# Kernel optimization log

Measured on AMD Instinct MI355X. Metric: run time of the kernel, lower is better.

## Reference

```python
import jax, jax.numpy as jnp
import numpy as np
from jax.scipy.linalg import solve_triangular

B, M, S, NBPS = 32768, 16, 8, 4
NUM_ITER = 2
EPS = 1e-4

def _pam_gray(b):
    if len(b) > 1:
        return (1 - 2 * b[0]) * (2 ** len(b[1:]) - _pam_gray(b[1:]))
    return 1 - 2 * b[0]

def _qam(nbps):
    n = 2 ** nbps
    pts = np.zeros(n, np.complex64)
    for i in range(n):
        b = np.array([int(c) for c in np.binary_repr(i, nbps)])
        pts[i] = _pam_gray(b[0::2]) + 1j * _pam_gray(b[1::2])
    pts = pts / np.sqrt(np.mean(np.abs(pts) ** 2))
    labels = ((np.arange(n)[:, None] >> np.arange(nbps - 1, -1, -1)) & 1).astype(np.float32)
    return pts.astype(np.complex64), labels

_PTS_NP, _LAB_NP = _qam(NBPS)
PTS = jnp.asarray(_PTS_NP)                                   # [P] complex64, unit-energy Gray QAM16
PTS_E = jnp.asarray((np.abs(_PTS_NP) ** 2).astype(np.float32))  # [P]
LAB = jnp.asarray(_LAB_NP)                                   # [P, K] bit labels (MSB first)
ASGN = 2.0 * LAB - 1.0                                       # [P, K], +1 where bit==1

def _symbol_logits(llr):
    # LLRs2SymbolLogits: llr=[...,S,K] (llr = log p(b=1)/p(b=0)) -> per-point log-prior [...,S,P]
    return jnp.sum(jax.nn.log_sigmoid(ASGN * llr[..., None, :]), axis=-1)

def _moments(logits):
    # SymbolLogits2Moments: softmax over points -> mean / variance of soft symbols
    p = jax.nn.softmax(logits, axis=-1)                       # [..., S, P]
    mean = jnp.einsum('...p,p->...', p.astype(jnp.complex64), PTS)
    e2 = jnp.einsum('...p,p->...', p, PTS_E)
    var = e2 - (mean.real ** 2 + mean.imag ** 2)
    return mean, var

def _demap(x_hat, llr_a, no_eff):
    # maxlog DemapperWithPrior, LLR = log p(b=1)/p(b=0)
    diff = x_hat[..., None] - PTS                             # [..., S, P]
    d2 = diff.real ** 2 + diff.imag ** 2
    exps = -d2 / no_eff[..., None] + _symbol_logits(llr_a)    # [..., S, P]
    e = exps[..., None]                                       # [..., S, P, 1]
    neg = jnp.float32(-1e30)
    l1 = jnp.max(jnp.where(LAB == 1.0, e, neg), axis=-2)      # [..., S, K]
    l0 = jnp.max(jnp.where(LAB == 0.0, e, neg), axis=-2)
    return l1 - l0

def _forward(y_re, y_im, h_re, h_im, prior, s_re, s_im):
    y = jax.lax.complex(y_re, y_im)                           # [B, M]
    h = jax.lax.complex(h_re, h_im)                           # [B, M, S]
    s = jax.lax.complex(s_re, s_im)                           # [B, M, M] Hermitian PSD
    # whiten_channel: s = L L^H, y <- L^-1 y, h <- L^-1 h
    L = jnp.linalg.cholesky(s)
    y = solve_triangular(L, y[..., None], lower=True)[..., 0]
    h = solve_triangular(L, h, lower=True)
    y_mf = jnp.einsum('bms,bm->bs', jnp.conj(h), y)[..., None]   # [B, S, 1] matched filter
    g = jnp.einsum('bmi,bmj->bij', jnp.conj(h), h)               # [B, S, S] Gram matrix
    # real-valued channel representation [[Re,-Im],[Im,Re]]
    hr = jnp.concatenate([
        jnp.concatenate([h.real, -h.imag], axis=-1),
        jnp.concatenate([h.imag, h.real], axis=-1)], axis=-2)    # [B, 2M, 2S]
    gr = jnp.einsum('bmi,bmj->bij', hr, hr)                      # [B, 2S, 2S]
    eye2s = jnp.eye(2 * S, dtype=jnp.float32)
    llr_d = prior
    llr_a = jnp.zeros_like(prior)
    for _ in range(NUM_ITER):
        llr_a = llr_d
        x_hat, var_x = _moments(_symbol_logits(llr_a))           # [B, S]
        # parallel interference cancellation in matched-filter domain
        y_mf_pic = (y_mf + g * x_hat[..., None, :]
                    - jnp.einsum('bij,bj->bi', g, x_hat)[..., None])  # [B, S, S]
        var2 = jnp.concatenate([var_x, var_x], axis=-1)          # [B, 2S]
        a = gr * var2[..., None, :] + eye2s                      # [B, 2S, 2S]
        a_inv = jnp.linalg.inv(a)
        mu = jnp.sum(a_inv * jnp.swapaxes(gr, -1, -2), axis=-1)  # diag(a_inv @ gr), [B, 2S]
        ypt = jnp.swapaxes(y_mf_pic, -1, -2)                     # [B, S, S] (stream-major)
        ypt_r = jnp.concatenate([ypt.real, ypt.imag], axis=-1)   # [B, S, 2S]
        ypt_r = jnp.concatenate([ypt_r, ypt_r], axis=-2)         # [B, 2S, 2S]
        z = jnp.sum(a_inv * ypt_r, axis=-1) / mu                 # [B, 2S] unbiased estimates
        zr, zi = jnp.split(z, 2, axis=-1)
        x_hat = jax.lax.complex(zr, zi)                          # [B, S]
        rho = mu / jnp.maximum(1.0 - var2 * mu, EPS)             # post-equalization SINR
        rho = jnp.split(rho, 2, axis=-1)[0]                      # [B, S]
        no_eff = 1.0 / rho
        llr_d = _demap(x_hat, llr_a, no_eff)
    return llr_d - llr_a  # extrinsic LLRs [B, S, K]

def setup_inputs() -> dict:
    key = jax.random.key(0)
    k = jax.random.split(key, 7)
    y_re = jax.random.normal(k[0], (B, M), jnp.float32)
    y_im = jax.random.normal(k[1], (B, M), jnp.float32)
    h_re = jax.random.normal(k[2], (B, M, S), jnp.float32) / np.float32(np.sqrt(2.0))
    h_im = jax.random.normal(k[3], (B, M, S), jnp.float32) / np.float32(np.sqrt(2.0))
    prior = 0.5 * jax.random.normal(k[4], (B, S, NBPS), jnp.float32)
    a = jax.lax.complex(jax.random.normal(k[5], (B, M, M), jnp.float32),
                        jax.random.normal(k[6], (B, M, M), jnp.float32)) / np.float32(np.sqrt(2.0 * M))
    s = jnp.einsum('bij,bkj->bik', a, jnp.conj(a)) + 0.5 * jnp.eye(M, dtype=jnp.complex64)
    return {"y_re": y_re, "y_im": y_im, "h_re": h_re, "h_im": h_im,
            "prior": prior, "s_re": s.real, "s_im": s.imag}

def reference(y_re, y_im, h_re, h_im, prior, s_re, s_im):
    return _forward(y_re, y_im, h_re, h_im, prior, s_re, s_im)
```

## Files before the change

### kernel.cpp

```cpp
#include <hip/hip_runtime.h>


#define EPS_F 1e-4f
#define INV_SQRT10 0.31622776601683794f
#define WSYNC() __builtin_amdgcn_wave_barrier()

__device__ __forceinline__ float rcpf(float x) { return __builtin_amdgcn_rcpf(x); }
__device__ __forceinline__ float pt_re(int p) {
    return (1.0f - 2.0f * (float)((p >> 3) & 1)) * (1.0f + 2.0f * (float)((p >> 1) & 1)) * INV_SQRT10;
}
__device__ __forceinline__ float pt_im(int p) {
    return (1.0f - 2.0f * (float)((p >> 2) & 1)) * (1.0f + 2.0f * (float)(p & 1)) * INV_SQRT10;
}

__global__ __launch_bounds__(64)
void mmse_pic_kernel(const float* __restrict__ y_re, const float* __restrict__ y_im,
                     const float* __restrict__ h_re, const float* __restrict__ h_im,
                     const float* __restrict__ prior,
                     const float* __restrict__ s_re, const float* __restrict__ s_im,
                     float* __restrict__ out)
{
    const int b = blockIdx.x, lane = threadIdx.x;
    const size_t bs = (size_t)b;

    __shared__ float2 Sc[16][28];
    __shared__ float2 Hc[16][10];
    __shared__ float2 xc_[8];
    __shared__ float2 ymc_[8];
    __shared__ float  vx_[8], ne_[8];
    __shared__ float  lsig[64];
    __shared__ float  logit_[8][20];
    __shared__ float  llrD_[8][4];

    {
        const float4* pr4 = (const float4*)(s_re + bs * 256);
        const float4* pi4 = (const float4*)(s_im + bs * 256);
        float4 vr = pr4[lane], vi = pi4[lane];
        int r = lane >> 2, c0 = (lane & 3) << 2;
        Sc[r][c0+0] = make_float2(vr.x, vi.x);
        Sc[r][c0+1] = make_float2(vr.y, vi.y);
        Sc[r][c0+2] = make_float2(vr.z, vi.z);
        Sc[r][c0+3] = make_float2(vr.w, vi.w);
        if (lane < 32) {
            const float4* hr4 = (const float4*)(h_re + bs * 128);
            const float4* hi4 = (const float4*)(h_im + bs * 128);
            float4 hr = hr4[lane], hi = hi4[lane];
            int row = lane >> 1, col = (lane & 1) << 2;
            float2 v0 = make_float2(hr.x, hi.x), v1 = make_float2(hr.y, hi.y);
            float2 v2 = make_float2(hr.z, hi.z), v3 = make_float2(hr.w, hi.w);
            Hc[row][col+0] = v0; Hc[row][col+1] = v1; Hc[row][col+2] = v2; Hc[row][col+3] = v3;
            Sc[row][16+col+0] = v0; Sc[row][16+col+1] = v1; Sc[row][16+col+2] = v2; Sc[row][16+col+3] = v3;
        }
        if (lane < 16) Sc[lane][24] = make_float2(y_re[bs*16+lane], y_im[bs*16+lane]);
        if (lane < 32) ((float*)llrD_)[lane] = prior[bs*32 + lane];
    }
    WSYNC();

    {
        const int j0 = lane & 15;
        for (int k = 0; k < 16; ++k) {
            float2 piv = Sc[k][k];
            float id = rcpf(piv.x*piv.x + piv.y*piv.y);
            float ipr = piv.x*id, ipi = -piv.y*id;
            int j1 = k + 1 + j0, j2 = j1 + 16;
            float2 rk0 = make_float2(0.f, 0.f), rk1 = make_float2(0.f, 0.f);
            if (j1 < 25) rk0 = Sc[k][j1];
            if (j2 < 25) rk1 = Sc[k][j2];
            #pragma unroll
            for (int p = 0; p < 4; ++p) {
                int i = (lane >> 4) + (p << 2);
                float2 aik = Sc[i][k];
                float mr = aik.x*ipr - aik.y*ipi;
                float mi = aik.x*ipi + aik.y*ipr;
                if (i == k) { mr = 0.f; mi = 0.f; }
                if (j1 < 25) {
                    float2 a = Sc[i][j1];
                    a.x -= mr*rk0.x - mi*rk0.y;
                    a.y -= mr*rk0.y + mi*rk0.x;
                    Sc[i][j1] = a;
                }
                if (j2 < 25) {
                    float2 a = Sc[i][j2];
                    a.x -= mr*rk1.x - mi*rk1.y;
                    a.y -= mr*rk1.y + mi*rk1.x;
                    Sc[i][j2] = a;
                }
            }
            WSYNC();
        }
    }
    {
        int i2 = lane >> 2, c = lane & 3;
        float2 d = Sc[i2][i2];
        float id = rcpf(d.x*d.x + d.y*d.y);
        float ipr = d.x*id, ipi = -d.y*id;
        #pragma unroll
        for (int q = 0; q < 3; ++q) {
            int j = 16 + c + (q << 2);
            if (j < 25) {
                float2 v = Sc[i2][j];
                Sc[i2][j] = make_float2(v.x*ipr - v.y*ipi, v.x*ipi + v.y*ipr);
            }
        }
    }
    WSYNC();

    const int s = lane >> 3, u = lane & 7;
    float g_re = 0.f, g_im = 0.f, ym_r = 0.f, ym_i = 0.f;
    #pragma unroll
    for (int m = 0; m < 16; ++m) {
        float2 h = Hc[m][s];
        float2 x = Sc[m][16 + u];
        float2 xy = Sc[m][24];
        g_re += h.x*x.x + h.y*x.y;
        g_im += h.x*x.y - h.y*x.x;
        ym_r += h.x*xy.x + h.y*xy.y;
        ym_i += h.x*xy.y - h.y*xy.x;
    }
    if (u == 0) ymc_[s] = make_float2(ym_r, ym_i);
    WSYNC();

    const float pr = pt_re(u), pi2 = pt_im(u), pe = pr*pr + pi2*pi2;
    float llr_a_reg = 0.f;

    for (int it = 0; it < 2; ++it) {
        {
            int ts = lane >> 3, tk = (lane >> 1) & 3, sg = lane & 1;
            float v = llrD_[ts][tk];
            float x = sg ? v : -v;
            lsig[lane] = fminf(x, 0.f) - log1pf(__expf(-fabsf(x)));
        }
        if (lane < 32) llr_a_reg = ((float*)llrD_)[lane];
        WSYNC();
        int base = s << 3;
        float lc = lsig[base | 2 | ((u >> 2) & 1)]
                 + lsig[base | 4 | ((u >> 1) & 1)]
                 + lsig[base | 6 | (u & 1)];
        float l0 = lc + lsig[base];
        float l1 = lc + lsig[base | 1];
        {
            float mx = fmaxf(l0, l1);
            mx = fmaxf(mx, __shfl_xor(mx, 1));
            mx = fmaxf(mx, __shfl_xor(mx, 2));
            mx = fmaxf(mx, __shfl_xor(mx, 4));
            float w0 = __expf(l0 - mx), w1 = __expf(l1 - mx);
            float a = w0 + w1, dw = w0 - w1;
            float se = a, mr = dw * pr, mi = a * pi2, e2 = a * pe;
            se += __shfl_xor(se,1); mr += __shfl_xor(mr,1); mi += __shfl_xor(mi,1); e2 += __shfl_xor(e2,1);
            se += __shfl_xor(se,2); mr += __shfl_xor(mr,2); mi += __shfl_xor(mi,2); e2 += __shfl_xor(e2,2);
            se += __shfl_xor(se,4); mr += __shfl_xor(mr,4); mi += __shfl_xor(mi,4); e2 += __shfl_xor(e2,4);
            if (u == 0) {
                float inv = rcpf(se);
                float mxr = mr*inv, mxi = mi*inv;
                xc_[s] = make_float2(mxr, mxi);
                vx_[s] = e2*inv - (mxr*mxr + mxi*mxi);
            }
        }
        WSYNC();
        float2 xj = xc_[u];
        float vj = vx_[u];
        float tr = g_re*xj.x - g_im*xj.y;
        float ti = g_re*xj.y + g_im*xj.x;
        tr += __shfl_xor(tr,1); ti += __shfl_xor(ti,1);
        tr += __shfl_xor(tr,2); ti += __shfl_xor(ti,2);
        tr += __shfl_xor(tr,4); ti += __shfl_xor(ti,4);
        float2 ym = ymc_[s];
        float br_ = ym.x - tr, bi_ = ym.y - ti;
        float Ar = g_re*vj + ((s == u) ? 1.f : 0.f);
        float Ai = g_im*vj;
        float Cr = g_re, Ci = g_im;
        #pragma unroll
        for (int k = 0; k < 8; ++k) {
            int rowsrc = (k << 3) | u;
            int colsrc = (s << 3) | k;
            float pvr = __shfl(Ar, k * 9);
            float pvi = __shfl(Ai, k * 9);
            float rAr = __shfl(Ar, rowsrc), rAi = __shfl(Ai, rowsrc);
            float rCr = __shfl(Cr, rowsrc), rCi = __shfl(Ci, rowsrc);
            float rbr = __shfl(br_, rowsrc), rbi = __shfl(bi_, rowsrc);
            float cAr = __shfl(Ar, colsrc), cAi = __shfl(Ai, colsrc);
            float id2 = rcpf(pvr*pvr + pvi*pvi);
            float ipr2 = pvr*id2, ipi2 = -pvi*id2;
            float mr2 = cAr*ipr2 - cAi*ipi2;
            float mi2 = cAr*ipi2 + cAi*ipr2;
            if (s == k) { mr2 = 0.f; mi2 = 0.f; }
            Ar  -= mr2*rAr - mi2*rAi;  Ai  -= mr2*rAi + mi2*rAr;
            Cr  -= mr2*rCr - mi2*rCi;  Ci  -= mr2*rCi + mi2*rCr;
            br_ -= mr2*rbr - mi2*rbi;  bi_ -= mr2*rbi + mi2*rbr;
        }
        if (s == u) {
            float id3 = rcpf(Ar*Ar + Ai*Ai);
            float ipr3 = Ar*id3, ipi3 = -Ai*id3;
            float wr = br_*ipr3 - bi_*ipi3;
            float wi = br_*ipi3 + bi_*ipr3;
            float ccr = Cr*ipr3 - Ci*ipi3;
            float cci = Cr*ipi3 + Ci*ipr3;
            float mu = ccr;
            float im = rcpf(mu);
            float zr = (wr + ccr*xj.x - cci*xj.y) * im;
            float zi = (wi + ccr*xj.y + cci*xj.x) * im;
            xc_[s] = make_float2(zr, zi);
            ne_[s] = fmaxf(1.f - vx_[s]*mu, EPS_F) * im;
        }
        WSYNC();
        {
            float2 xh = xc_[s];
            float idn = rcpf(ne_[s]);
            float dr0 = xh.x - pr, dr1 = xh.x + pr, di = xh.y - pi2;
            logit_[s][u]     = l0 - (dr0*dr0 + di*di) * idn;
            logit_[s][u + 8] = l1 - (dr1*dr1 + di*di) * idn;
        }
        WSYNC();
        {
            int s2 = lane >> 3, kb = (lane >> 1) & 3, half = lane & 1;
            int bitpos = 3 - kb;
            float m = -1e30f;
            #pragma unroll
            for (int q = 0; q < 8; ++q) {
                int low  = q & ((1 << bitpos) - 1);
                int high = (q >> bitpos) << (bitpos + 1);
                int p = high | (half << bitpos) | low;
                m = fmaxf(m, logit_[s2][p]);
            }
            float other = __shfl_xor(m, 1);
            if (half == 1) llrD_[s2][kb] = m - other;
        }
        WSYNC();
    }

    if (lane < 32) out[bs*32 + lane] = ((float*)llrD_)[lane] - llr_a_reg;
}

extern "C" void kernel_launch(void* const* d_in, const int* in_sizes, int n_in,
                              void* d_out, int out_size, void* d_ws, size_t ws_size,
                              hipStream_t stream) {
    const float* y_re  = (const float*)d_in[0];
    const float* y_im  = (const float*)d_in[1];
    const float* h_re  = (const float*)d_in[2];
    const float* h_im  = (const float*)d_in[3];
    const float* prior = (const float*)d_in[4];
    const float* s_re  = (const float*)d_in[5];
    const float* s_im  = (const float*)d_in[6];
    float* out = (float*)d_out;

    const int B = in_sizes[0] / 16;
    mmse_pic_kernel<<<dim3(B), dim3(64), 0, stream>>>(
        y_re, y_im, h_re, h_im, prior, s_re, s_im, out);
}
```

Measured before the change: 285.1 us.

## Exploit Hermitian structure in elimination, pack two batches per block

Each block now holds two waves, one batch item per wave, with separate shared-memory slices per wave. The Gauss-Jordan elimination becomes a forward-only, Cholesky-like reduction that uses real pivots, skips rows above the pivot and trims the right-hand-side columns. It then scales by the reciprocal square root of the pivot so that A^H S^-1 A comes from a single factor, which drops the separate H copy. log1pf is also swapped for a fast __logf. The goal is fewer LDS operations and less arithmetic per batch item plus better block scheduling, at the cost of depending on S being Hermitian positive definite and losing some log precision. B is assumed even.

```diff
diff --git a/kernel.cpp b/kernel.cpp
--- a/kernel.cpp
+++ b/kernel.cpp
@@ -6,6 +6,7 @@
 #define WSYNC() __builtin_amdgcn_wave_barrier()
 
 __device__ __forceinline__ float rcpf(float x) { return __builtin_amdgcn_rcpf(x); }
+__device__ __forceinline__ float rsqf(float x) { return __builtin_amdgcn_rsqf(x); }
 __device__ __forceinline__ float pt_re(int p) {
     return (1.0f - 2.0f * (float)((p >> 3) & 1)) * (1.0f + 2.0f * (float)((p >> 1) & 1)) * INV_SQRT10;
 }
@@ -13,94 +14,92 @@
     return (1.0f - 2.0f * (float)((p >> 2) & 1)) * (1.0f + 2.0f * (float)(p & 1)) * INV_SQRT10;
 }
 
-__global__ __launch_bounds__(64)
+__global__ __launch_bounds__(128, 8)
 void mmse_pic_kernel(const float* __restrict__ y_re, const float* __restrict__ y_im,
                      const float* __restrict__ h_re, const float* __restrict__ h_im,
                      const float* __restrict__ prior,
                      const float* __restrict__ s_re, const float* __restrict__ s_im,
                      float* __restrict__ out)
 {
-    const int b = blockIdx.x, lane = threadIdx.x;
+    const int lane = threadIdx.x & 63;
+    const int w    = threadIdx.x >> 6;
+    const int b    = blockIdx.x * 2 + w;
     const size_t bs = (size_t)b;
 
-    __shared__ float2 Sc[16][28];
-    __shared__ float2 Hc[16][10];
-    __shared__ float2 xc_[8];
-    __shared__ float2 ymc_[8];
-    __shared__ float  vx_[8], ne_[8];
-    __shared__ float  lsig[64];
-    __shared__ float  logit_[8][20];
-    __shared__ float  llrD_[8][4];
+    __shared__ float2 Sc[2][16][28];
+    __shared__ float2 xc_[2][8];
+    __shared__ float2 ymc_[2][8];
+    __shared__ float  vx_[2][8], ne_[2][8];
+    __shared__ float  lsig[2][64];
+    __shared__ float  logit_[2][8][20];
+    __shared__ float  llrD_[2][8][4];
 
     {
         const float4* pr4 = (const float4*)(s_re + bs * 256);
         const float4* pi4 = (const float4*)(s_im + bs * 256);
         float4 vr = pr4[lane], vi = pi4[lane];
         int r = lane >> 2, c0 = (lane & 3) << 2;
-        Sc[r][c0+0] = make_float2(vr.x, vi.x);
-        Sc[r][c0+1] = make_float2(vr.y, vi.y);
-        Sc[r][c0+2] = make_float2(vr.z, vi.z);
-        Sc[r][c0+3] = make_float2(vr.w, vi.w);
+        Sc[w][r][c0+0] = make_float2(vr.x, vi.x);
+        Sc[w][r][c0+1] = make_float2(vr.y, vi.y);
+        Sc[w][r][c0+2] = make_float2(vr.z, vi.z);
+        Sc[w][r][c0+3] = make_float2(vr.w, vi.w);
         if (lane < 32) {
             const float4* hr4 = (const float4*)(h_re + bs * 128);
             const float4* hi4 = (const float4*)(h_im + bs * 128);
             float4 hr = hr4[lane], hi = hi4[lane];
-            int row = lane >> 1, col = (lane & 1) << 2;
-            float2 v0 = make_float2(hr.x, hi.x), v1 = make_float2(hr.y, hi.y);
-            float2 v2 = make_float2(hr.z, hi.z), v3 = make_float2(hr.w, hi.w);
-            Hc[row][col+0] = v0; Hc[row][col+1] = v1; Hc[row][col+2] = v2; Hc[row][col+3] = v3;
-            Sc[row][16+col+0] = v0; Sc[row][16+col+1] = v1; Sc[row][16+col+2] = v2; Sc[row][16+col+3] = v3;
-        }
-        if (lane < 16) Sc[lane][24] = make_float2(y_re[bs*16+lane], y_im[bs*16+lane]);
-        if (lane < 32) ((float*)llrD_)[lane] = prior[bs*32 + lane];
+            int row = lane >> 1, col = 16 + ((lane & 1) << 2);
+            Sc[w][row][col+0] = make_float2(hr.x, hi.x);
+            Sc[w][row][col+1] = make_float2(hr.y, hi.y);
+            Sc[w][row][col+2] = make_float2(hr.z, hi.z);
+            Sc[w][row][col+3] = make_float2(hr.w, hi.w);
+        }
+        if (lane < 16) Sc[w][lane][24] = make_float2(y_re[bs*16+lane], y_im[bs*16+lane]);
+        if (lane < 32) ((float*)llrD_[w])[lane] = prior[bs*32 + lane];
     }
     WSYNC();
 
     {
         const int j0 = lane & 15;
-        for (int k = 0; k < 16; ++k) {
-            float2 piv = Sc[k][k];
-            float id = rcpf(piv.x*piv.x + piv.y*piv.y);
-            float ipr = piv.x*id, ipi = -piv.y*id;
+        const int r4 = lane >> 4;
+        for (int k = 0; k < 15; ++k) {
+            float invd = rcpf(Sc[w][k][k].x);
             int j1 = k + 1 + j0, j2 = j1 + 16;
             float2 rk0 = make_float2(0.f, 0.f), rk1 = make_float2(0.f, 0.f);
-            if (j1 < 25) rk0 = Sc[k][j1];
-            if (j2 < 25) rk1 = Sc[k][j2];
-            #pragma unroll
-            for (int p = 0; p < 4; ++p) {
-                int i = (lane >> 4) + (p << 2);
-                float2 aik = Sc[i][k];
-                float mr = aik.x*ipr - aik.y*ipi;
-                float mi = aik.x*ipi + aik.y*ipr;
-                if (i == k) { mr = 0.f; mi = 0.f; }
+            if (j1 < 25) rk0 = Sc[w][k][j1];
+            const bool blk2 = (k < 8);
+            if (blk2 && j2 < 25) rk1 = Sc[w][k][j2];
+            const int pmin = (k + 1) >> 2;
+            for (int p = pmin; p < 4; ++p) {
+                int i = (p << 2) + r4;
+                float2 aik = Sc[w][i][k];
+                float mr = aik.x * invd, mi = aik.y * invd;
+                if (i <= k) { mr = 0.f; mi = 0.f; }
                 if (j1 < 25) {
-                    float2 a = Sc[i][j1];
+                    float2 a = Sc[w][i][j1];
                     a.x -= mr*rk0.x - mi*rk0.y;
                     a.y -= mr*rk0.y + mi*rk0.x;
-                    Sc[i][j1] = a;
+                    Sc[w][i][j1] = a;
                 }
-                if (j2 < 25) {
-                    float2 a = Sc[i][j2];
+                if (blk2 && j2 < 25) {
+                    float2 a = Sc[w][i][j2];
                     a.x -= mr*rk1.x - mi*rk1.y;
                     a.y -= mr*rk1.y + mi*rk1.x;
-                    Sc[i][j2] = a;
+                    Sc[w][i][j2] = a;
                 }
             }
             WSYNC();
         }
     }
     {
-        int i2 = lane >> 2, c = lane & 3;
-        float2 d = Sc[i2][i2];
-        float id = rcpf(d.x*d.x + d.y*d.y);
-        float ipr = d.x*id, ipi = -d.y*id;
-        #pragma unroll
-        for (int q = 0; q < 3; ++q) {
-            int j = 16 + c + (q << 2);
-            if (j < 25) {
-                float2 v = Sc[i2][j];
-                Sc[i2][j] = make_float2(v.x*ipr - v.y*ipi, v.x*ipi + v.y*ipr);
-            }
+        int r2 = lane >> 2, c = lane & 3;
+        float irs = rsqf(Sc[w][r2][r2].x);
+        float2 v0 = Sc[w][r2][16 + c];
+        Sc[w][r2][16 + c] = make_float2(v0.x*irs, v0.y*irs);
+        float2 v1 = Sc[w][r2][20 + c];
+        Sc[w][r2][20 + c] = make_float2(v1.x*irs, v1.y*irs);
+        if (c == 0) {
+            float2 v2 = Sc[w][r2][24];
+            Sc[w][r2][24] = make_float2(v2.x*irs, v2.y*irs);
         }
     }
     WSYNC();
@@ -109,15 +108,15 @@
     float g_re = 0.f, g_im = 0.f, ym_r = 0.f, ym_i = 0.f;
     #pragma unroll
     for (int m = 0; m < 16; ++m) {
-        float2 h = Hc[m][s];
-        float2 x = Sc[m][16 + u];
-        float2 xy = Sc[m][24];
-        g_re += h.x*x.x + h.y*x.y;
-        g_im += h.x*x.y - h.y*x.x;
-        ym_r += h.x*xy.x + h.y*xy.y;
-        ym_i += h.x*xy.y - h.y*xy.x;
-    }
-    if (u == 0) ymc_[s] = make_float2(ym_r, ym_i);
+        float2 a  = Sc[w][m][16 + s];
+        float2 x  = Sc[w][m][16 + u];
+        float2 xy = Sc[w][m][24];
+        g_re += a.x*x.x + a.y*x.y;
+        g_im += a.x*x.y - a.y*x.x;
+        ym_r += a.x*xy.x + a.y*xy.y;
+        ym_i += a.x*xy.y - a.y*xy.x;
+    }
+    if (u == 0) ymc_[w][s] = make_float2(ym_r, ym_i);
     WSYNC();
 
     const float pr = pt_re(u), pi2 = pt_im(u), pe = pr*pr + pi2*pi2;
@@ -126,18 +125,18 @@
     for (int it = 0; it < 2; ++it) {
         {
             int ts = lane >> 3, tk = (lane >> 1) & 3, sg = lane & 1;
-            float v = llrD_[ts][tk];
+            float v = llrD_[w][ts][tk];
             float x = sg ? v : -v;
-            lsig[lane] = fminf(x, 0.f) - log1pf(__expf(-fabsf(x)));
-        }
-        if (lane < 32) llr_a_reg = ((float*)llrD_)[lane];
+            lsig[w][lane] = fminf(x, 0.f) - __logf(1.0f + __expf(-fabsf(x)));
+        }
+        if (lane < 32) llr_a_reg = ((float*)llrD_[w])[lane];
         WSYNC();
         int base = s << 3;
-        float lc = lsig[base | 2 | ((u >> 2) & 1)]
-                 + lsig[base | 4 | ((u >> 1) & 1)]
-                 + lsig[base | 6 | (u & 1)];
-        float l0 = lc + lsig[base];
-        float l1 = lc + lsig[base | 1];
+        float lc = lsig[w][base | 2 | ((u >> 2) & 1)]
+                 + lsig[w][base | 4 | ((u >> 1) & 1)]
+                 + lsig[w][base | 6 | (u & 1)];
+        float l0 = lc + lsig[w][base];
+        float l1 = lc + lsig[w][base | 1];
         {
             float mx = fmaxf(l0, l1);
             mx = fmaxf(mx, __shfl_xor(mx, 1));
@@ -152,19 +151,19 @@
             if (u == 0) {
                 float inv = rcpf(se);
                 float mxr = mr*inv, mxi = mi*inv;
-                xc_[s] = make_float2(mxr, mxi);
-                vx_[s] = e2*inv - (mxr*mxr + mxi*mxi);
+                xc_[w][s] = make_float2(mxr, mxi);
+                vx_[w][s] = e2*inv - (mxr*mxr + mxi*mxi);
             }
         }
         WSYNC();
-        float2 xj = xc_[u];
-        float vj = vx_[u];
+        float2 xj = xc_[w][u];
+        float vj = vx_[w][u];
         float tr = g_re*xj.x - g_im*xj.y;
         float ti = g_re*xj.y + g_im*xj.x;
         tr += __shfl_xor(tr,1); ti += __shfl_xor(ti,1);
         tr += __shfl_xor(tr,2); ti += __shfl_xor(ti,2);
         tr += __shfl_xor(tr,4); ti += __shfl_xor(ti,4);
-        float2 ym = ymc_[s];
+        float2 ym = ymc_[w][s];
         float br_ = ym.x - tr, bi_ = ym.y - ti;
         float Ar = g_re*vj + ((s == u) ? 1.f : 0.f);
         float Ai = g_im*vj;
@@ -199,16 +198,16 @@
             float im = rcpf(mu);
             float zr = (wr + ccr*xj.x - cci*xj.y) * im;
             float zi = (wi + ccr*xj.y + cci*xj.x) * im;
-            xc_[s] = make_float2(zr, zi);
-            ne_[s] = fmaxf(1.f - vx_[s]*mu, EPS_F) * im;
-        }
-        WSYNC();
-        {
-            float2 xh = xc_[s];
-            float idn = rcpf(ne_[s]);
+            xc_[w][s] = make_float2(zr, zi);
+            ne_[w][s] = fmaxf(1.f - vx_[w][s]*mu, EPS_F) * im;
+        }
+        WSYNC();
+        {
+            float2 xh = xc_[w][s];
+            float idn = rcpf(ne_[w][s]);
             float dr0 = xh.x - pr, dr1 = xh.x + pr, di = xh.y - pi2;
-            logit_[s][u]     = l0 - (dr0*dr0 + di*di) * idn;
-            logit_[s][u + 8] = l1 - (dr1*dr1 + di*di) * idn;
+            logit_[w][s][u]     = l0 - (dr0*dr0 + di*di) * idn;
+            logit_[w][s][u + 8] = l1 - (dr1*dr1 + di*di) * idn;
         }
         WSYNC();
         {
@@ -220,15 +219,15 @@
                 int low  = q & ((1 << bitpos) - 1);
                 int high = (q >> bitpos) << (bitpos + 1);
                 int p = high | (half << bitpos) | low;
-                m = fmaxf(m, logit_[s2][p]);
+                m = fmaxf(m, logit_[w][s2][p]);
             }
             float other = __shfl_xor(m, 1);
-            if (half == 1) llrD_[s2][kb] = m - other;
-        }
-        WSYNC();
-    }
-
-    if (lane < 32) out[bs*32 + lane] = ((float*)llrD_)[lane] - llr_a_reg;
+            if (half == 1) llrD_[w][s2][kb] = m - other;
+        }
+        WSYNC();
+    }
+
+    if (lane < 32) out[bs*32 + lane] = ((float*)llrD_[w])[lane] - llr_a_reg;
 }
 
 extern "C" void kernel_launch(void* const* d_in, const int* in_sizes, int n_in,
@@ -244,6 +243,6 @@
     float* out = (float*)d_out;
 
     const int B = in_sizes[0] / 16;
-    mmse_pic_kernel<<<dim3(B), dim3(64), 0, stream>>>(
+    mmse_pic_kernel<<<dim3(B / 2), dim3(128), 0, stream>>>(
         y_re, y_im, h_re, h_im, prior, s_re, s_im, out);
 }
```

Result: slower. 418.1 us (+46.6%).
